# Kernel optimization log

Measured on AMD Instinct MI355X. Metric: run time of the kernel, lower is better.

## Reference

```python
import jax, jax.numpy as jnp
import numpy as np

B = 256          # batch
H = 1024         # conditioning_size (dec_hid_dim)
D = 256          # gst_dim
G = 32           # num_gst
C = 16           # num_cells
O = 256          # output_size


def setup_inputs() -> dict:
    key = jax.random.key(0)
    ks = jax.random.split(key, 7)
    hidden = jax.random.normal(ks[0], (B, H), dtype=jnp.float32)
    # per-cell embedding tables: nn.Embedding(num_gst, gst_dim) stacked over cells
    gst_emb = jax.random.normal(ks[1], (C, G, D), dtype=jnp.float32)
    # per-cell Linear(gst_dim + cond, cond): weight [H, H + D] (torch [out, in]), bias [H]
    attn_w = jax.random.normal(ks[2], (C, H, H + D), dtype=jnp.float32) * 0.02
    attn_b = jax.random.normal(ks[3], (C, H), dtype=jnp.float32) * 0.02
    # per-cell v: Parameter(torch.rand(cond))
    v = jax.random.uniform(ks[4], (C, H), dtype=jnp.float32)
    # out Linear(gst_dim, output_size)
    out_w = jax.random.normal(ks[5], (O, D), dtype=jnp.float32) * 0.02
    out_b = jax.random.normal(ks[6], (O,), dtype=jnp.float32) * 0.02
    return {"hidden": hidden, "gst_emb": gst_emb, "attn_w": attn_w,
            "attn_b": attn_b, "v": v, "out_w": out_w, "out_b": out_b}


def reference(hidden, gst_emb, attn_w, attn_b, v, out_w, out_b):
    # Original concatenates (hidden, encoder_outputs) along features; split the
    # linear weight accordingly instead of materializing the concat.
    w_hid = attn_w[:, :, :H]        # [C, H, H]
    w_enc = attn_w[:, :, H:]        # [C, H, D]
    # embedding lookup of arange(G) == the table rows themselves (same for all batch)
    enc = gst_emb                   # [C, G, D]
    hid_part = jnp.einsum('bh,coh->bco', hidden, w_hid)     # [B, C, Ho]
    enc_part = jnp.einsum('cgd,cod->cgo', enc, w_enc)       # [C, G, Ho]
    energy = jnp.tanh(hid_part[:, :, None, :] + enc_part[None]
                      + attn_b[None, :, None, :])           # [B, C, G, Ho]
    scores = jnp.einsum('bcgh,ch->bcg', energy, v)          # [B, C, G]
    attention = jax.nn.softmax(scores, axis=-1)             # softmax over num_gst
    weighted = jnp.einsum('bcg,cgd->bcd', attention, enc)   # [B, C, D]
    att_cat = attention.reshape(B, C * G)                   # torch.cat(att_list, dim=1)
    pooled = jnp.mean(weighted, axis=1)                     # [B, D]
    out = pooled @ out_w.T + out_b                          # [B, O]
    return (att_cat, out)
```

## Files before the change

kernel.cpp:

```cpp
#include <hip/hip_runtime.h>
#include <hip/hip_bf16.h>

#define B_  256
#define H_  1024
#define D_  256
#define G_  32
#define C_  16
#define O_  256
#define HD_ 1280
#define N1_ 16384
#define RS_ 40

typedef __attribute__((ext_vector_type(8)))  short short8;
typedef __attribute__((ext_vector_type(4)))  short s16x4;
typedef __attribute__((ext_vector_type(4)))  float f32x4;
typedef __attribute__((ext_vector_type(16))) float f32x16;

#define MFMA32(a, b, c) __builtin_amdgcn_mfma_f32_32x32x16_bf16((a), (b), (c), 0, 0, 0)

__device__ __forceinline__ float tanh_c(float x) {
    float y = __expf(2.f * x);
    float t = 1.f - 2.f * __builtin_amdgcn_rcpf(y + 1.f);
    return fminf(fmaxf(t, -0.99999994f), 0.99999994f);
}

__device__ __forceinline__ short bfhi(float x) {
    return (short)(__float_as_uint(x) >> 16);
}
__device__ __forceinline__ short bflo(float x) {
    float fhi = __uint_as_float(__float_as_uint(x) & 0xFFFF0000u);
    return (short)(__float_as_uint(x - fhi) >> 16);
}

__device__ __forceinline__ void split4(const float4 v, s16x4& hi, s16x4& lo) {
    hi[0] = bfhi(v.x); lo[0] = bflo(v.x);
    hi[1] = bfhi(v.y); lo[1] = bflo(v.y);
    hi[2] = bfhi(v.z); lo[2] = bflo(v.z);
    hi[3] = bfhi(v.w); lo[3] = bflo(v.w);
}

__global__ __launch_bounds__(256, 2) void gemm1_kernel(
    const short* __restrict__ hidH, const short* __restrict__ hidL,
    const float* __restrict__ attn_w, const float* __restrict__ attn_b,
    float* __restrict__ hp)
{
    __shared__ short AsH[2][128 * RS_];
    __shared__ short AsL[2][128 * RS_];
    __shared__ short BsH[2][64 * RS_];
    __shared__ short BsL[2][64 * RS_];

    const int tid  = threadIdx.x;
    const int wave = tid >> 6, lane = tid & 63;
    const int m0 = blockIdx.x * 128;
    const int n0 = blockIdx.y * 64;
    const int wm = (wave >> 1) * 64;
    const int wn = (wave & 1) * 32;
    const int l31 = lane & 31;
    const int kh  = (lane >> 5) * 8;

    f32x16 acc0, acc1;
    #pragma unroll
    for (int i = 0; i < 16; ++i) { acc0[i] = 0.f; acc1[i] = 0.f; }

    const int rA = tid >> 2, cA = (tid & 3) * 8;
    const int rB = tid >> 3, cB = (tid & 7) * 4;
    const short* pAH0 = hidH + (size_t)(m0 + rA) * H_ + cA;
    const short* pAH1 = pAH0 + 64 * H_;
    const short* pAL0 = hidL + (size_t)(m0 + rA) * H_ + cA;
    const short* pAL1 = pAL0 + 64 * H_;
    const float* pB0  = attn_w + (size_t)(n0 + rB) * HD_ + cB;
    const float* pB1  = pB0 + (size_t)32 * HD_;

    const int wA0 = rA * RS_ + cA, wA1 = wA0 + 64 * RS_;
    const int wB0 = rB * RS_ + cB, wB1 = wB0 + 32 * RS_;
    const int aoff0 = (wm + l31) * RS_ + kh;
    const int aoff1 = aoff0 + 32 * RS_;
    const int boff  = (wn + l31) * RS_ + kh;

    short8 raH[2][2], raL[2][2];
    float4 rb[2][2];

    raH[0][0] = *(const short8*)(pAH0);       raH[0][1] = *(const short8*)(pAH1);
    raL[0][0] = *(const short8*)(pAL0);       raL[0][1] = *(const short8*)(pAL1);
    rb[0][0]  = *(const float4*)(pB0);        rb[0][1]  = *(const float4*)(pB1);
    raH[1][0] = *(const short8*)(pAH0 + 32);  raH[1][1] = *(const short8*)(pAH1 + 32);
    raL[1][0] = *(const short8*)(pAL0 + 32);  raL[1][1] = *(const short8*)(pAL1 + 32);
    rb[1][0]  = *(const float4*)(pB0 + 32);   rb[1][1]  = *(const float4*)(pB1 + 32);

    *(short8*)(&AsH[0][wA0]) = raH[0][0];
    *(short8*)(&AsH[0][wA1]) = raH[0][1];
    *(short8*)(&AsL[0][wA0]) = raL[0][0];
    *(short8*)(&AsL[0][wA1]) = raL[0][1];
    {   s16x4 h_, l_;
        split4(rb[0][0], h_, l_);
        *(s16x4*)(&BsH[0][wB0]) = h_; *(s16x4*)(&BsL[0][wB0]) = l_;
        split4(rb[0][1], h_, l_);
        *(s16x4*)(&BsH[0][wB1]) = h_; *(s16x4*)(&BsL[0][wB1]) = l_;
    }
    raH[0][0] = *(const short8*)(pAH0 + 64);  raH[0][1] = *(const short8*)(pAH1 + 64);
    raL[0][0] = *(const short8*)(pAL0 + 64);  raL[0][1] = *(const short8*)(pAL1 + 64);
    rb[0][0]  = *(const float4*)(pB0 + 64);   rb[0][1]  = *(const float4*)(pB1 + 64);

    asm volatile("s_waitcnt lgkmcnt(0)" ::: "memory");
    __builtin_amdgcn_s_barrier();

#define SLAB(P, DOW, DOL, KL, DOB)                                            \
    {                                                                         \
        if (DOW) {                                                            \
            *(short8*)(&AsH[P ^ 1][wA0]) = raH[P ^ 1][0];                     \
            *(short8*)(&AsH[P ^ 1][wA1]) = raH[P ^ 1][1];                     \
            *(short8*)(&AsL[P ^ 1][wA0]) = raL[P ^ 1][0];                     \
            *(short8*)(&AsL[P ^ 1][wA1]) = raL[P ^ 1][1];                     \
            s16x4 h_, l_;                                                     \
            split4(rb[P ^ 1][0], h_, l_);                                     \
            *(s16x4*)(&BsH[P ^ 1][wB0]) = h_;                                 \
            *(s16x4*)(&BsL[P ^ 1][wB0]) = l_;                                 \
            split4(rb[P ^ 1][1], h_, l_);                                     \
            *(s16x4*)(&BsH[P ^ 1][wB1]) = h_;                                 \
            *(s16x4*)(&BsL[P ^ 1][wB1]) = l_;                                 \
        }                                                                     \
        if (DOL) {                                                            \
            raH[P ^ 1][0] = *(const short8*)(pAH0 + (KL));                    \
            raH[P ^ 1][1] = *(const short8*)(pAH1 + (KL));                    \
            raL[P ^ 1][0] = *(const short8*)(pAL0 + (KL));                    \
            raL[P ^ 1][1] = *(const short8*)(pAL1 + (KL));                    \
            rb[P ^ 1][0]  = *(const float4*)(pB0 + (KL));                     \
            rb[P ^ 1][1]  = *(const float4*)(pB1 + (KL));                     \
        }                                                                     \
        _Pragma("unroll")                                                     \
        for (int ks = 0; ks < 2; ++ks) {                                      \
            short8 ah0 = *(const short8*)(&AsH[P][aoff0 + ks * 16]);          \
            short8 ah1 = *(const short8*)(&AsH[P][aoff1 + ks * 16]);          \
            short8 al0 = *(const short8*)(&AsL[P][aoff0 + ks * 16]);          \
            short8 al1 = *(const short8*)(&AsL[P][aoff1 + ks * 16]);          \
            short8 bh  = *(const short8*)(&BsH[P][boff + ks * 16]);           \
            short8 bl  = *(const short8*)(&BsL[P][boff + ks * 16]);           \
            acc0 = MFMA32(ah0, bh, acc0);                                     \
            acc1 = MFMA32(ah1, bh, acc1);                                     \
            acc0 = MFMA32(al0, bh, acc0);                                     \
            acc1 = MFMA32(al1, bh, acc1);                                     \
            acc0 = MFMA32(ah0, bl, acc0);                                     \
            acc1 = MFMA32(ah1, bl, acc1);                                     \
        }                                                                     \
        if (DOB) {                                                            \
            asm volatile("s_waitcnt lgkmcnt(0)" ::: "memory");                \
            __builtin_amdgcn_s_barrier();                                     \
        }                                                                     \
    }

    for (int S = 0; S < 28; S += 2) {
        SLAB(0, 1, 1, (S + 3) * 32, 1)
        SLAB(1, 1, 1, (S + 4) * 32, 1)
    }
    SLAB(0, 1, 1, 31 * 32, 1)
    SLAB(1, 1, 0, 0, 1)
    SLAB(0, 1, 0, 0, 1)
    SLAB(1, 0, 0, 0, 0)
#undef SLAB

    const int col  = n0 + wn + l31;
    const float bias = attn_b[col];
    const int rbase = m0 + wm + (lane >> 5) * 4;
    float* dcol = hp + col;
    #pragma unroll
    for (int r = 0; r < 16; ++r) {
        const int row = rbase + (r & 3) + 8 * (r >> 2);
        dcol[(size_t)row * N1_]        = tanh_c(acc0[r] + bias);
        dcol[(size_t)(row + 32) * N1_] = tanh_c(acc1[r] + bias);
    }
}

__global__ __launch_bounds__(256) void gemm2_kernel(
    const float* __restrict__ enc, const float* __restrict__ attn_w,
    const float* __restrict__ hidden, float* __restrict__ ep,
    short* __restrict__ hidH, short* __restrict__ hidL)
{
    const int tid  = threadIdx.x;
    const int wave = tid >> 6, lane = tid & 63;

    {
        const int base = (blockIdx.y * 16 + blockIdx.x) * 1024 + tid * 4;
        const float4 h4 = *(const float4*)(hidden + base);
        s16x4 hh, ll;
        split4(h4, hh, ll);
        *(s16x4*)(hidH + base) = hh;
        *(s16x4*)(hidL + base) = ll;
    }

    const int c  = blockIdx.y;
    const int n0 = blockIdx.x * 64 + wave * 16;
    const int l16 = lane & 15;
    const int lk  = (lane >> 4) * 8;

#define MFMA16(a, b, c) __builtin_amdgcn_mfma_f32_16x16x32_bf16((a), (b), (c), 0, 0, 0)
    f32x4 acc[2];
    acc[0] = f32x4{0.f, 0.f, 0.f, 0.f};
    acc[1] = f32x4{0.f, 0.f, 0.f, 0.f};

    const float* encp = enc + c * (G_ * D_);
    const float* wp   = attn_w + (size_t)c * H_ * HD_ + H_;

    #pragma unroll
    for (int kk = 0; kk < 8; ++kk) {
        const int k0 = kk * 32 + lk;
        short8 ah[2], al[2], bh, bl;
        #pragma unroll
        for (int mi = 0; mi < 2; ++mi) {
            const float* p = encp + (mi * 16 + l16) * D_ + k0;
            s16x4 h0, l0, h1, l1;
            split4(*(const float4*)p, h0, l0);
            split4(*(const float4*)(p + 4), h1, l1);
            ah[mi] = short8{h0[0],h0[1],h0[2],h0[3],h1[0],h1[1],h1[2],h1[3]};
            al[mi] = short8{l0[0],l0[1],l0[2],l0[3],l1[0],l1[1],l1[2],l1[3]};
        }
        {
            const float* p = wp + (size_t)(n0 + l16) * HD_ + k0;
            s16x4 h0, l0, h1, l1;
            split4(*(const float4*)p, h0, l0);
            split4(*(const float4*)(p + 4), h1, l1);
            bh = short8{h0[0],h0[1],h0[2],h0[3],h1[0],h1[1],h1[2],h1[3]};
            bl = short8{l0[0],l0[1],l0[2],l0[3],l1[0],l1[1],l1[2],l1[3]};
        }
        #pragma unroll
        for (int mi = 0; mi < 2; ++mi) {
            acc[mi] = MFMA16(ah[mi], bh, acc[mi]);
            acc[mi] = MFMA16(al[mi], bh, acc[mi]);
            acc[mi] = MFMA16(ah[mi], bl, acc[mi]);
        }
    }

    const int lr = (lane >> 4) * 4;
    #pragma unroll
    for (int mi = 0; mi < 2; ++mi) {
        const int g = mi * 16 + lr;
        const int o = n0 + l16;
        float* dst = ep + (c * G_ + g) * H_ + o;
        f32x4 vacc = acc[mi];
        dst[0]      = tanh_c(vacc[0]);
        dst[H_]     = tanh_c(vacc[1]);
        dst[2 * H_] = tanh_c(vacc[2]);
        dst[3 * H_] = tanh_c(vacc[3]);
    }
#undef MFMA16
}

__global__ __launch_bounds__(256) void attn_kernel(
    const float* __restrict__ hp, const float* __restrict__ ep,
    const float* __restrict__ v, const float* __restrict__ enc,
    float* __restrict__ out, float* __restrict__ wt)
{
    const int c  = blockIdx.x;
    const int b0 = blockIdx.y * 4;
    const int tid  = threadIdx.x;
    const int wave = tid >> 6, lane = tid & 63;

    __shared__ float s_att[4][G_];
    __shared__ float s_sc[4][G_];

    f32x4 vv[4], tav[4][4];
    const float* vrow = v + c * H_;
    #pragma unroll
    for (int j = 0; j < 4; ++j)
        vv[j] = *(const f32x4*)(vrow + lane * 4 + j * 256);
    #pragma unroll
    for (int bi = 0; bi < 4; ++bi) {
        const float* hprow = hp + (size_t)(b0 + bi) * N1_ + c * H_;
        #pragma unroll
        for (int j = 0; j < 4; ++j)
            tav[bi][j] = *(const f32x4*)(hprow + lane * 4 + j * 256);
    }

    #pragma unroll
    for (int gg = 0; gg < 8; ++gg) {
        const int g = wave * 8 + gg;
        const float* eprow = ep + (size_t)(c * G_ + g) * H_;
        float s[4] = {0.f, 0.f, 0.f, 0.f};
        #pragma unroll
        for (int j = 0; j < 4; ++j) {
            const f32x4 tb = *(const f32x4*)(eprow + lane * 4 + j * 256);
            #pragma unroll
            for (int e = 0; e < 4; ++e) {
                const float tbx = tb[e];
                const float w   = vv[j][e];
                #pragma unroll
                for (int bi = 0; bi < 4; ++bi) {
                    const float ta  = tav[bi][j][e];
                    const float num = ta + tbx;
                    const float den = fmaf(ta, tbx, 1.f);
                    s[bi] = fmaf(num * __builtin_amdgcn_rcpf(den), w, s[bi]);
                }
            }
        }
        #pragma unroll
        for (int off = 32; off > 0; off >>= 1) {
            s[0] += __shfl_down(s[0], off, 64);
            s[1] += __shfl_down(s[1], off, 64);
            s[2] += __shfl_down(s[2], off, 64);
            s[3] += __shfl_down(s[3], off, 64);
        }
        if (lane == 0) {
            s_sc[0][g] = s[0]; s_sc[1][g] = s[1];
            s_sc[2][g] = s[2]; s_sc[3][g] = s[3];
        }
    }
    __syncthreads();

    if (tid < 128) {
        const int bi = tid >> 5, g = tid & 31;
        float sv = s_sc[bi][g];
        float m = sv;
        #pragma unroll
        for (int off = 16; off > 0; off >>= 1)
            m = fmaxf(m, __shfl_xor(m, off, 32));
        const float e = __expf(sv - m);
        float sum = e;
        #pragma unroll
        for (int off = 16; off > 0; off >>= 1)
            sum += __shfl_xor(sum, off, 32);
        const float a = e / sum;
        s_att[bi][g] = a;
        out[(size_t)(b0 + bi) * (C_ * G_) + c * G_ + g] = a;
    }
    __syncthreads();

    float w0 = 0.f, w1 = 0.f, w2 = 0.f, w3 = 0.f;
    const float* encc = enc + c * (G_ * D_) + tid;
    #pragma unroll
    for (int g = 0; g < G_; ++g) {
        const float e = encc[g * D_];
        w0 = fmaf(s_att[0][g], e, w0);
        w1 = fmaf(s_att[1][g], e, w1);
        w2 = fmaf(s_att[2][g], e, w2);
        w3 = fmaf(s_att[3][g], e, w3);
    }
    wt[(size_t)((b0 + 0) * C_ + c) * D_ + tid] = w0;
    wt[(size_t)((b0 + 1) * C_ + c) * D_ + tid] = w1;
    wt[(size_t)((b0 + 2) * C_ + c) * D_ + tid] = w2;
    wt[(size_t)((b0 + 3) * C_ + c) * D_ + tid] = w3;
}

__global__ __launch_bounds__(256) void out_kernel(
    const float* __restrict__ wt, const float* __restrict__ out_w,
    const float* __restrict__ out_b, float* __restrict__ out)
{
    const int b = blockIdx.x, tid = threadIdx.x;
    __shared__ float pooled[D_];

    float s = 0.f;
    #pragma unroll
    for (int c = 0; c < C_; ++c)
        s += wt[(size_t)(b * C_ + c) * D_ + tid];
    pooled[tid] = s * (1.f / 16.f);
    __syncthreads();

    float acc = out_b[tid];
    const float* wrow = out_w + tid * D_;
    #pragma unroll 8
    for (int dc = 0; dc < 64; ++dc) {
        float4 w4 = *(const float4*)(wrow + dc * 4);
        acc += pooled[dc * 4 + 0] * w4.x;
        acc += pooled[dc * 4 + 1] * w4.y;
        acc += pooled[dc * 4 + 2] * w4.z;
        acc += pooled[dc * 4 + 3] * w4.w;
    }
    out[(size_t)B_ * (C_ * G_) + b * O_ + tid] = acc;
}

extern "C" void kernel_launch(void* const* d_in, const int* in_sizes, int n_in,
                              void* d_out, int out_size, void* d_ws, size_t ws_size,
                              hipStream_t stream) {
    const float* hidden = (const float*)d_in[0];
    const float* enc    = (const float*)d_in[1];
    const float* attn_w = (const float*)d_in[2];
    const float* attn_b = (const float*)d_in[3];
    const float* v      = (const float*)d_in[4];
    const float* out_w  = (const float*)d_in[5];
    const float* out_b  = (const float*)d_in[6];
    float* out = (float*)d_out;

    float* hp = (float*)d_ws;
    float* ep = hp + (size_t)B_ * N1_;
    float* wt = ep + (size_t)C_ * G_ * H_;
    short* hidH = (short*)(wt + (size_t)B_ * C_ * D_);
    short* hidL = hidH + (size_t)B_ * H_;

    gemm2_kernel<<<dim3(16, C_), 256, 0, stream>>>(enc, attn_w, hidden, ep, hidH, hidL);
    gemm1_kernel<<<dim3(2, 256), 256, 0, stream>>>(hidH, hidL, attn_w, attn_b, hp);
    attn_kernel<<<dim3(C_, B_ / 4), 256, 0, stream>>>(hp, ep, v, enc, out, wt);
    out_kernel<<<B_, 256, 0, stream>>>(wt, out_w, out_b, out);
}
```

Baseline: 213.3 us.

## Single-buffer LDS in gemm1 and raise occupancy to four blocks per CU

Replaces the double-buffered shared-memory ping-pong pipeline in gemm1 with a single LDS buffer and a single register prefetch stage, and raises launch bounds from 2 to 4 blocks per SM. The aim is to halve LDS and register use so more blocks can be resident and hide latency through occupancy instead of software pipelining. In exchange each K-step now needs two barriers, and the LDS writes are serialized with the MFMA reads.

```diff
diff --git a/kernel.cpp b/kernel.cpp
--- a/kernel.cpp
+++ b/kernel.cpp
@@ -39,15 +39,15 @@
     hi[3] = bfhi(v.w); lo[3] = bflo(v.w);
 }
 
-__global__ __launch_bounds__(256, 2) void gemm1_kernel(
+__global__ __launch_bounds__(256, 4) void gemm1_kernel(
     const short* __restrict__ hidH, const short* __restrict__ hidL,
     const float* __restrict__ attn_w, const float* __restrict__ attn_b,
     float* __restrict__ hp)
 {
-    __shared__ short AsH[2][128 * RS_];
-    __shared__ short AsL[2][128 * RS_];
-    __shared__ short BsH[2][64 * RS_];
-    __shared__ short BsL[2][64 * RS_];
+    __shared__ short AsH[128 * RS_];
+    __shared__ short AsL[128 * RS_];
+    __shared__ short BsH[64 * RS_];
+    __shared__ short BsL[64 * RS_];
 
     const int tid  = threadIdx.x;
     const int wave = tid >> 6, lane = tid & 63;
@@ -77,86 +77,67 @@
     const int aoff1 = aoff0 + 32 * RS_;
     const int boff  = (wn + l31) * RS_ + kh;
 
-    short8 raH[2][2], raL[2][2];
-    float4 rb[2][2];
-
-    raH[0][0] = *(const short8*)(pAH0);       raH[0][1] = *(const short8*)(pAH1);
-    raL[0][0] = *(const short8*)(pAL0);       raL[0][1] = *(const short8*)(pAL1);
-    rb[0][0]  = *(const float4*)(pB0);        rb[0][1]  = *(const float4*)(pB1);
-    raH[1][0] = *(const short8*)(pAH0 + 32);  raH[1][1] = *(const short8*)(pAH1 + 32);
-    raL[1][0] = *(const short8*)(pAL0 + 32);  raL[1][1] = *(const short8*)(pAL1 + 32);
-    rb[1][0]  = *(const float4*)(pB0 + 32);   rb[1][1]  = *(const float4*)(pB1 + 32);
-
-    *(short8*)(&AsH[0][wA0]) = raH[0][0];
-    *(short8*)(&AsH[0][wA1]) = raH[0][1];
-    *(short8*)(&AsL[0][wA0]) = raL[0][0];
-    *(short8*)(&AsL[0][wA1]) = raL[0][1];
-    {   s16x4 h_, l_;
-        split4(rb[0][0], h_, l_);
-        *(s16x4*)(&BsH[0][wB0]) = h_; *(s16x4*)(&BsL[0][wB0]) = l_;
-        split4(rb[0][1], h_, l_);
-        *(s16x4*)(&BsH[0][wB1]) = h_; *(s16x4*)(&BsL[0][wB1]) = l_;
-    }
-    raH[0][0] = *(const short8*)(pAH0 + 64);  raH[0][1] = *(const short8*)(pAH1 + 64);
-    raL[0][0] = *(const short8*)(pAL0 + 64);  raL[0][1] = *(const short8*)(pAL1 + 64);
-    rb[0][0]  = *(const float4*)(pB0 + 64);   rb[0][1]  = *(const float4*)(pB1 + 64);
-
+    short8 rH0, rH1, rL0, rL1;
+    float4 rb0, rb1;
+
+#define STAGE_WRITE()                                                         \
+    {                                                                         \
+        *(short8*)(&AsH[wA0]) = rH0;                                          \
+        *(short8*)(&AsH[wA1]) = rH1;                                          \
+        *(short8*)(&AsL[wA0]) = rL0;                                          \
+        *(short8*)(&AsL[wA1]) = rL1;                                          \
+        s16x4 h_, l_;                                                         \
+        split4(rb0, h_, l_);                                                  \
+        *(s16x4*)(&BsH[wB0]) = h_;                                            \
+        *(s16x4*)(&BsL[wB0]) = l_;                                            \
+        split4(rb1, h_, l_);                                                  \
+        *(s16x4*)(&BsH[wB1]) = h_;                                            \
+        *(s16x4*)(&BsL[wB1]) = l_;                                            \
+    }
+
+#define STAGE_LOAD(KOFF)                                                      \
+    {                                                                         \
+        rH0 = *(const short8*)(pAH0 + (KOFF));                                \
+        rH1 = *(const short8*)(pAH1 + (KOFF));                                \
+        rL0 = *(const short8*)(pAL0 + (KOFF));                                \
+        rL1 = *(const short8*)(pAL1 + (KOFF));                                \
+        rb0 = *(const float4*)(pB0 + (KOFF));                                 \
+        rb1 = *(const float4*)(pB1 + (KOFF));                                 \
+    }
+
+    STAGE_LOAD(0)
+    STAGE_WRITE()
+    STAGE_LOAD(32)
     asm volatile("s_waitcnt lgkmcnt(0)" ::: "memory");
     __builtin_amdgcn_s_barrier();
 
-#define SLAB(P, DOW, DOL, KL, DOB)                                            \
-    {                                                                         \
-        if (DOW) {                                                            \
-            *(short8*)(&AsH[P ^ 1][wA0]) = raH[P ^ 1][0];                     \
-            *(short8*)(&AsH[P ^ 1][wA1]) = raH[P ^ 1][1];                     \
-            *(short8*)(&AsL[P ^ 1][wA0]) = raL[P ^ 1][0];                     \
-            *(short8*)(&AsL[P ^ 1][wA1]) = raL[P ^ 1][1];                     \
-            s16x4 h_, l_;                                                     \
-            split4(rb[P ^ 1][0], h_, l_);                                     \
-            *(s16x4*)(&BsH[P ^ 1][wB0]) = h_;                                 \
-            *(s16x4*)(&BsL[P ^ 1][wB0]) = l_;                                 \
-            split4(rb[P ^ 1][1], h_, l_);                                     \
-            *(s16x4*)(&BsH[P ^ 1][wB1]) = h_;                                 \
-            *(s16x4*)(&BsL[P ^ 1][wB1]) = l_;                                 \
-        }                                                                     \
-        if (DOL) {                                                            \
-            raH[P ^ 1][0] = *(const short8*)(pAH0 + (KL));                    \
-            raH[P ^ 1][1] = *(const short8*)(pAH1 + (KL));                    \
-            raL[P ^ 1][0] = *(const short8*)(pAL0 + (KL));                    \
-            raL[P ^ 1][1] = *(const short8*)(pAL1 + (KL));                    \
-            rb[P ^ 1][0]  = *(const float4*)(pB0 + (KL));                     \
-            rb[P ^ 1][1]  = *(const float4*)(pB1 + (KL));                     \
-        }                                                                     \
-        _Pragma("unroll")                                                     \
-        for (int ks = 0; ks < 2; ++ks) {                                      \
-            short8 ah0 = *(const short8*)(&AsH[P][aoff0 + ks * 16]);          \
-            short8 ah1 = *(const short8*)(&AsH[P][aoff1 + ks * 16]);          \
-            short8 al0 = *(const short8*)(&AsL[P][aoff0 + ks * 16]);          \
-            short8 al1 = *(const short8*)(&AsL[P][aoff1 + ks * 16]);          \
-            short8 bh  = *(const short8*)(&BsH[P][boff + ks * 16]);           \
-            short8 bl  = *(const short8*)(&BsL[P][boff + ks * 16]);           \
-            acc0 = MFMA32(ah0, bh, acc0);                                     \
-            acc1 = MFMA32(ah1, bh, acc1);                                     \
-            acc0 = MFMA32(al0, bh, acc0);                                     \
-            acc1 = MFMA32(al1, bh, acc1);                                     \
-            acc0 = MFMA32(ah0, bl, acc0);                                     \
-            acc1 = MFMA32(ah1, bl, acc1);                                     \
-        }                                                                     \
-        if (DOB) {                                                            \
-            asm volatile("s_waitcnt lgkmcnt(0)" ::: "memory");                \
-            __builtin_amdgcn_s_barrier();                                     \
-        }                                                                     \
-    }
-
-    for (int S = 0; S < 28; S += 2) {
-        SLAB(0, 1, 1, (S + 3) * 32, 1)
-        SLAB(1, 1, 1, (S + 4) * 32, 1)
-    }
-    SLAB(0, 1, 1, 31 * 32, 1)
-    SLAB(1, 1, 0, 0, 1)
-    SLAB(0, 1, 0, 0, 1)
-    SLAB(1, 0, 0, 0, 0)
-#undef SLAB
+    for (int k = 0; k < 32; ++k) {
+        #pragma unroll
+        for (int ks = 0; ks < 2; ++ks) {
+            short8 ah0 = *(const short8*)(&AsH[aoff0 + ks * 16]);
+            short8 ah1 = *(const short8*)(&AsH[aoff1 + ks * 16]);
+            short8 al0 = *(const short8*)(&AsL[aoff0 + ks * 16]);
+            short8 al1 = *(const short8*)(&AsL[aoff1 + ks * 16]);
+            short8 bh  = *(const short8*)(&BsH[boff + ks * 16]);
+            short8 bl  = *(const short8*)(&BsL[boff + ks * 16]);
+            acc0 = MFMA32(ah0, bh, acc0);
+            acc1 = MFMA32(ah1, bh, acc1);
+            acc0 = MFMA32(al0, bh, acc0);
+            acc1 = MFMA32(al1, bh, acc1);
+            acc0 = MFMA32(ah0, bl, acc0);
+            acc1 = MFMA32(ah1, bl, acc1);
+        }
+        if (k < 31) {
+            asm volatile("s_waitcnt lgkmcnt(0)" ::: "memory");
+            __builtin_amdgcn_s_barrier();
+            STAGE_WRITE()
+            if (k < 30) STAGE_LOAD((k + 2) * 32)
+            asm volatile("s_waitcnt lgkmcnt(0)" ::: "memory");
+            __builtin_amdgcn_s_barrier();
+        }
+    }
+#undef STAGE_WRITE
+#undef STAGE_LOAD
 
     const int col  = n0 + wn + l31;
     const float bias = attn_b[col];
```

Result: no change. 215.6 us (+1.1%).

## Pre-swizzle hidden into MFMA fragment layout and load A directly to registers

Applied to the files above, without the earlier changes.

The bf16 hi/lo split of hidden is now written in a layout that matches MFMA fragment order, so gemm1 reads its A operand straight from global memory into registers and no longer stages it in LDS. Each block now covers all 256 batch rows by 32 output columns, so the attn_w tile is read and split only once per column slice instead of twice. MFMA sections are wrapped in s_setprio. The aim is less LDS traffic and fewer redundant weight reads; the cost is more register pressure and reliance on L2 for the repeated hidden reads.

```diff
diff --git a/kernel.cpp b/kernel.cpp
--- a/kernel.cpp
+++ b/kernel.cpp
@@ -44,17 +44,12 @@
     const float* __restrict__ attn_w, const float* __restrict__ attn_b,
     float* __restrict__ hp)
 {
-    __shared__ short AsH[2][128 * RS_];
-    __shared__ short AsL[2][128 * RS_];
-    __shared__ short BsH[2][64 * RS_];
-    __shared__ short BsL[2][64 * RS_];
+    __shared__ short BsH[2][32 * RS_];
+    __shared__ short BsL[2][32 * RS_];
 
     const int tid  = threadIdx.x;
     const int wave = tid >> 6, lane = tid & 63;
-    const int m0 = blockIdx.x * 128;
-    const int n0 = blockIdx.y * 64;
-    const int wm = (wave >> 1) * 64;
-    const int wn = (wave & 1) * 32;
+    const int n0  = blockIdx.x * 32;
     const int l31 = lane & 31;
     const int kh  = (lane >> 5) * 8;
 
@@ -62,85 +57,74 @@
     #pragma unroll
     for (int i = 0; i < 16; ++i) { acc0[i] = 0.f; acc1[i] = 0.f; }
 
-    const int rA = tid >> 2, cA = (tid & 3) * 8;
     const int rB = tid >> 3, cB = (tid & 7) * 4;
-    const short* pAH0 = hidH + (size_t)(m0 + rA) * H_ + cA;
-    const short* pAH1 = pAH0 + 64 * H_;
-    const short* pAL0 = hidL + (size_t)(m0 + rA) * H_ + cA;
-    const short* pAL1 = pAL0 + 64 * H_;
-    const float* pB0  = attn_w + (size_t)(n0 + rB) * HD_ + cB;
-    const float* pB1  = pB0 + (size_t)32 * HD_;
-
-    const int wA0 = rA * RS_ + cA, wA1 = wA0 + 64 * RS_;
-    const int wB0 = rB * RS_ + cB, wB1 = wB0 + 32 * RS_;
-    const int aoff0 = (wm + l31) * RS_ + kh;
-    const int aoff1 = aoff0 + 32 * RS_;
-    const int boff  = (wn + l31) * RS_ + kh;
-
-    short8 raH[2][2], raL[2][2];
-    float4 rb[2][2];
-
-    raH[0][0] = *(const short8*)(pAH0);       raH[0][1] = *(const short8*)(pAH1);
-    raL[0][0] = *(const short8*)(pAL0);       raL[0][1] = *(const short8*)(pAL1);
-    rb[0][0]  = *(const float4*)(pB0);        rb[0][1]  = *(const float4*)(pB1);
-    raH[1][0] = *(const short8*)(pAH0 + 32);  raH[1][1] = *(const short8*)(pAH1 + 32);
-    raL[1][0] = *(const short8*)(pAL0 + 32);  raL[1][1] = *(const short8*)(pAL1 + 32);
-    rb[1][0]  = *(const float4*)(pB0 + 32);   rb[1][1]  = *(const float4*)(pB1 + 32);
-
-    *(short8*)(&AsH[0][wA0]) = raH[0][0];
-    *(short8*)(&AsH[0][wA1]) = raH[0][1];
-    *(short8*)(&AsL[0][wA0]) = raL[0][0];
-    *(short8*)(&AsL[0][wA1]) = raL[0][1];
-    {   s16x4 h_, l_;
-        split4(rb[0][0], h_, l_);
-        *(s16x4*)(&BsH[0][wB0]) = h_; *(s16x4*)(&BsL[0][wB0]) = l_;
-        split4(rb[0][1], h_, l_);
-        *(s16x4*)(&BsH[0][wB1]) = h_; *(s16x4*)(&BsL[0][wB1]) = l_;
-    }
-    raH[0][0] = *(const short8*)(pAH0 + 64);  raH[0][1] = *(const short8*)(pAH1 + 64);
-    raL[0][0] = *(const short8*)(pAL0 + 64);  raL[0][1] = *(const short8*)(pAL1 + 64);
-    rb[0][0]  = *(const float4*)(pB0 + 64);   rb[0][1]  = *(const float4*)(pB1 + 64);
-
+    const float* pB = attn_w + (size_t)(n0 + rB) * HD_ + cB;
+    const int wB = rB * RS_ + cB;
+    const int boff = l31 * RS_ + kh;
+
+    const size_t aBase = (size_t)(wave * 2) * 32768 + (size_t)lane * 8;
+    const short* pH0 = hidH + aBase;
+    const short* pH1 = hidH + aBase + 32768;
+    const short* pL0 = hidL + aBase;
+    const short* pL1 = hidL + aBase + 32768;
+
+    float4 rb[2];
+    short8 aH0[2][2], aH1[2][2], aL0[2][2], aL1[2][2];
+
+    rb[0] = *(const float4*)(pB);
+    {   s16x4 h_, l_; split4(rb[0], h_, l_);
+        *(s16x4*)(&BsH[0][wB]) = h_;
+        *(s16x4*)(&BsL[0][wB]) = l_; }
+    rb[1] = *(const float4*)(pB + 32);
+    aH0[0][0] = *(const short8*)(pH0);
+    aH0[0][1] = *(const short8*)(pH0 + 512);
+    aH1[0][0] = *(const short8*)(pH1);
+    aH1[0][1] = *(const short8*)(pH1 + 512);
+    aL0[0][0] = *(const short8*)(pL0);
+    aL0[0][1] = *(const short8*)(pL0 + 512);
+    aL1[0][0] = *(const short8*)(pL1);
+    aL1[0][1] = *(const short8*)(pL1 + 512);
     asm volatile("s_waitcnt lgkmcnt(0)" ::: "memory");
     __builtin_amdgcn_s_barrier();
 
-#define SLAB(P, DOW, DOL, KL, DOB)                                            \
+#define BODY(P, K0, DOW, DOLB, DOLA, DOB)                                     \
     {                                                                         \
         if (DOW) {                                                            \
-            *(short8*)(&AsH[P ^ 1][wA0]) = raH[P ^ 1][0];                     \
-            *(short8*)(&AsH[P ^ 1][wA1]) = raH[P ^ 1][1];                     \
-            *(short8*)(&AsL[P ^ 1][wA0]) = raL[P ^ 1][0];                     \
-            *(short8*)(&AsL[P ^ 1][wA1]) = raL[P ^ 1][1];                     \
             s16x4 h_, l_;                                                     \
-            split4(rb[P ^ 1][0], h_, l_);                                     \
-            *(s16x4*)(&BsH[P ^ 1][wB0]) = h_;                                 \
-            *(s16x4*)(&BsL[P ^ 1][wB0]) = l_;                                 \
-            split4(rb[P ^ 1][1], h_, l_);                                     \
-            *(s16x4*)(&BsH[P ^ 1][wB1]) = h_;                                 \
-            *(s16x4*)(&BsL[P ^ 1][wB1]) = l_;                                 \
+            split4(rb[P ^ 1], h_, l_);                                        \
+            *(s16x4*)(&BsH[P ^ 1][wB]) = h_;                                  \
+            *(s16x4*)(&BsL[P ^ 1][wB]) = l_;                                  \
         }                                                                     \
-        if (DOL) {                                                            \
-            raH[P ^ 1][0] = *(const short8*)(pAH0 + (KL));                    \
-            raH[P ^ 1][1] = *(const short8*)(pAH1 + (KL));                    \
-            raL[P ^ 1][0] = *(const short8*)(pAL0 + (KL));                    \
-            raL[P ^ 1][1] = *(const short8*)(pAL1 + (KL));                    \
-            rb[P ^ 1][0]  = *(const float4*)(pB0 + (KL));                     \
-            rb[P ^ 1][1]  = *(const float4*)(pB1 + (KL));                     \
+        if (DOLB) rb[P] = *(const float4*)(pB + ((K0) + 2) * 32);             \
+        if (DOLA) {                                                           \
+            aH0[P ^ 1][0] = *(const short8*)(pH0 + ((K0) + 1) * 1024);        \
+            aH0[P ^ 1][1] = *(const short8*)(pH0 + ((K0) + 1) * 1024 + 512);  \
+            aH1[P ^ 1][0] = *(const short8*)(pH1 + ((K0) + 1) * 1024);        \
+            aH1[P ^ 1][1] = *(const short8*)(pH1 + ((K0) + 1) * 1024 + 512);  \
+            aL0[P ^ 1][0] = *(const short8*)(pL0 + ((K0) + 1) * 1024);        \
+            aL0[P ^ 1][1] = *(const short8*)(pL0 + ((K0) + 1) * 1024 + 512);  \
+            aL1[P ^ 1][0] = *(const short8*)(pL1 + ((K0) + 1) * 1024);        \
+            aL1[P ^ 1][1] = *(const short8*)(pL1 + ((K0) + 1) * 1024 + 512);  \
         }                                                                     \
-        _Pragma("unroll")                                                     \
-        for (int ks = 0; ks < 2; ++ks) {                                      \
-            short8 ah0 = *(const short8*)(&AsH[P][aoff0 + ks * 16]);          \
-            short8 ah1 = *(const short8*)(&AsH[P][aoff1 + ks * 16]);          \
-            short8 al0 = *(const short8*)(&AsL[P][aoff0 + ks * 16]);          \
-            short8 al1 = *(const short8*)(&AsL[P][aoff1 + ks * 16]);          \
-            short8 bh  = *(const short8*)(&BsH[P][boff + ks * 16]);           \
-            short8 bl  = *(const short8*)(&BsL[P][boff + ks * 16]);           \
-            acc0 = MFMA32(ah0, bh, acc0);                                     \
-            acc1 = MFMA32(ah1, bh, acc1);                                     \
-            acc0 = MFMA32(al0, bh, acc0);                                     \
-            acc1 = MFMA32(al1, bh, acc1);                                     \
-            acc0 = MFMA32(ah0, bl, acc0);                                     \
-            acc1 = MFMA32(ah1, bl, acc1);                                     \
+        {                                                                     \
+            short8 bh0 = *(const short8*)(&BsH[P][boff]);                     \
+            short8 bl0 = *(const short8*)(&BsL[P][boff]);                     \
+            short8 bh1 = *(const short8*)(&BsH[P][boff + 16]);                \
+            short8 bl1 = *(const short8*)(&BsL[P][boff + 16]);                \
+            __builtin_amdgcn_s_setprio(1);                                    \
+            acc0 = MFMA32(aH0[P][0], bh0, acc0);                              \
+            acc1 = MFMA32(aH1[P][0], bh0, acc1);                              \
+            acc0 = MFMA32(aL0[P][0], bh0, acc0);                              \
+            acc1 = MFMA32(aL1[P][0], bh0, acc1);                              \
+            acc0 = MFMA32(aH0[P][0], bl0, acc0);                              \
+            acc1 = MFMA32(aH1[P][0], bl0, acc1);                              \
+            acc0 = MFMA32(aH0[P][1], bh1, acc0);                              \
+            acc1 = MFMA32(aH1[P][1], bh1, acc1);                              \
+            acc0 = MFMA32(aL0[P][1], bh1, acc0);                              \
+            acc1 = MFMA32(aL1[P][1], bh1, acc1);                              \
+            acc0 = MFMA32(aH0[P][1], bl1, acc0);                              \
+            acc1 = MFMA32(aH1[P][1], bl1, acc1);                              \
+            __builtin_amdgcn_s_setprio(0);                                    \
         }                                                                     \
         if (DOB) {                                                            \
             asm volatile("s_waitcnt lgkmcnt(0)" ::: "memory");                \
@@ -148,19 +132,17 @@
         }                                                                     \
     }
 
-    for (int S = 0; S < 28; S += 2) {
-        SLAB(0, 1, 1, (S + 3) * 32, 1)
-        SLAB(1, 1, 1, (S + 4) * 32, 1)
-    }
-    SLAB(0, 1, 1, 31 * 32, 1)
-    SLAB(1, 1, 0, 0, 1)
-    SLAB(0, 1, 0, 0, 1)
-    SLAB(1, 0, 0, 0, 0)
-#undef SLAB
-
-    const int col  = n0 + wn + l31;
+    for (int k0 = 0; k0 < 30; k0 += 2) {
+        BODY(0, k0, 1, 1, 1, 1)
+        BODY(1, k0 + 1, 1, 1, 1, 1)
+    }
+    BODY(0, 30, 1, 0, 1, 1)
+    BODY(1, 31, 0, 0, 0, 0)
+#undef BODY
+
+    const int col  = n0 + l31;
     const float bias = attn_b[col];
-    const int rbase = m0 + wm + (lane >> 5) * 4;
+    const int rbase = wave * 64 + (lane >> 5) * 4;
     float* dcol = hp + col;
     #pragma unroll
     for (int r = 0; r < 16; ++r) {
@@ -179,12 +161,24 @@
     const int wave = tid >> 6, lane = tid & 63;
 
     {
-        const int base = (blockIdx.y * 16 + blockIdx.x) * 1024 + tid * 4;
-        const float4 h4 = *(const float4*)(hidden + base);
-        s16x4 hh, ll;
-        split4(h4, hh, ll);
-        *(s16x4*)(hidH + base) = hh;
-        *(s16x4*)(hidL + base) = ll;
+        const int bid = blockIdx.y * 16 + blockIdx.x;
+        const int gid = bid * 256 + tid;
+        if (gid < 32768) {
+            const int s   = gid >> 12;
+            const int k0  = (gid >> 7) & 31;
+            const int ks  = (gid >> 6) & 1;
+            const int ln  = gid & 63;
+            const int row = s * 32 + (ln & 31);
+            const int colk = k0 * 32 + ks * 16 + (ln >> 5) * 8;
+            const float* src = hidden + (size_t)row * H_ + colk;
+            s16x4 h0, l0, h1, l1;
+            split4(*(const float4*)src, h0, l0);
+            split4(*(const float4*)(src + 4), h1, l1);
+            *(short8*)(hidH + (size_t)gid * 8) =
+                short8{h0[0],h0[1],h0[2],h0[3],h1[0],h1[1],h1[2],h1[3]};
+            *(short8*)(hidL + (size_t)gid * 8) =
+                short8{l0[0],l0[1],l0[2],l0[3],l1[0],l1[1],l1[2],l1[3]};
+        }
     }
 
     const int c  = blockIdx.y;
@@ -385,7 +379,7 @@
     short* hidL = hidH + (size_t)B_ * H_;
 
     gemm2_kernel<<<dim3(16, C_), 256, 0, stream>>>(enc, attn_w, hidden, ep, hidH, hidL);
-    gemm1_kernel<<<dim3(2, 256), 256, 0, stream>>>(hidH, hidL, attn_w, attn_b, hp);
+    gemm1_kernel<<<512, 256, 0, stream>>>(hidH, hidL, attn_w, attn_b, hp);
     attn_kernel<<<dim3(C_, B_ / 4), 256, 0, stream>>>(hp, ep, v, enc, out, wt);
     out_kernel<<<B_, 256, 0, stream>>>(wt, out_w, out_b, out);
 }
```

Result: faster. 205.4 us (-3.7%).
